# Optimization experiments

Measured on AMD Instinct MI355X. Metric: run time of the kernel, lower is better.

The kernel has to match this reference:

```python
import jax, jax.numpy as jnp
import numpy as np

D_MODEL = 768
N_HEADS = 12
HEAD_DIM = D_MODEL // N_HEADS
NEG = -10000.0


def setup_inputs() -> dict:
    key = jax.random.key(0)
    ks = jax.random.split(key, 8)
    B, S, D = 2, 2048, D_MODEL
    inp = {
        "q": jax.random.normal(ks[0], (B, S, D), dtype=jnp.float32),
        "k": jax.random.normal(ks[1], (B, S, D), dtype=jnp.float32),
        "v": jax.random.normal(ks[2], (B, S, D), dtype=jnp.float32),
        "attn_mask": jax.random.randint(ks[3], (B, S), 0, 2, dtype=jnp.int32),
        # weights stored [in, out]; apply as x @ W (equivalent to torch Linear)
        "Wq": jax.random.normal(ks[4], (D, D), dtype=jnp.float32) / np.sqrt(D),
        "Wk": jax.random.normal(ks[5], (D, D), dtype=jnp.float32) / np.sqrt(D),
        "Wv": jax.random.normal(ks[6], (D, D), dtype=jnp.float32) / np.sqrt(D),
        "Wo": jax.random.normal(ks[7], (D, D), dtype=jnp.float32) / np.sqrt(D),
        "mask_future": 1,
    }
    return inp


def reference(q, k, v, attn_mask, Wq, Wk, Wv, Wo, mask_future):
    B, S, D = q.shape
    H, hd = N_HEADS, HEAD_DIM
    # project and split heads -> [B, H, S, hd]
    qh = (q @ Wq).reshape(B, S, H, hd).transpose(0, 2, 1, 3)
    kh = (k @ Wk).reshape(B, S, H, hd).transpose(0, 2, 1, 3)
    vh = (v @ Wv).reshape(B, S, H, hd).transpose(0, 2, 1, 3)

    scale = 1.0 / np.sqrt(hd).astype(np.float32)
    # full [B, H, L, S] score matrix (naive SDPA, as in the original)
    scores = jnp.einsum("bhld,bhsd->bhls", qh, kh) * scale
    if mask_future:
        causal = jnp.triu(jnp.full((S, S), NEG, dtype=scores.dtype), k=1)
        scores = scores + causal
    # padding mask: [B, S] -> broadcast over heads and query positions
    pad = attn_mask[:, None, None, :] == 0
    scores = jnp.where(pad, NEG, scores)
    attn = jax.nn.softmax(scores, axis=-1)  # dropout p=0.0 -> identity
    out = jnp.einsum("bhls,bhsd->bhld", attn, vh)  # [B, H, L, hd]
    out = out.transpose(0, 2, 1, 3).reshape(B, S, D)
    return out @ Wo
```

## Files before the change

kernel.cpp:

```cpp
#include <hip/hip_runtime.h>


#define NEGV (-10000.0f)

typedef __attribute__((ext_vector_type(8))) short v8s;
typedef __attribute__((ext_vector_type(4))) float v4f;
typedef __attribute__((ext_vector_type(8))) unsigned short v8u;

__device__ __forceinline__ unsigned short f2bf(float f) {
  unsigned int u = __float_as_uint(f);
  u += 0x7FFFu + ((u >> 16) & 1u);
  return (unsigned short)(u >> 16);
}

__global__ __launch_bounds__(256) void transpose_w(
    const float* __restrict__ w0, const float* __restrict__ w1,
    const float* __restrict__ w2, const float* __restrict__ w3,
    unsigned short* __restrict__ t0, unsigned short* __restrict__ t1,
    unsigned short* __restrict__ t2, unsigned short* __restrict__ t3) {
  const float* w; unsigned short* t;
  switch (blockIdx.z) {
    case 0: w = w0; t = t0; break;
    case 1: w = w1; t = t1; break;
    case 2: w = w2; t = t2; break;
    default: w = w3; t = t3; break;
  }
  __shared__ unsigned short tile[32][33];
  const int tx = threadIdx.x & 31, ty = threadIdx.x >> 5;
  const int x0 = blockIdx.x * 32, y0 = blockIdx.y * 32;
#pragma unroll
  for (int j = 0; j < 4; j++)
    tile[ty + j * 8][tx] = f2bf(w[(size_t)(y0 + ty + j * 8) * 768 + x0 + tx]);
  __syncthreads();
#pragma unroll
  for (int j = 0; j < 4; j++)
    t[(size_t)(x0 + ty + j * 8) * 768 + y0 + tx] = tile[tx][ty + j * 8];
}

template <bool ABF16HEAD, bool CF32ROW>
__device__ __forceinline__ void gemm_core(const void* __restrict__ A,
                                          const unsigned short* __restrict__ Wt,
                                          void* __restrict__ C) {
  const int tid = threadIdx.x;
  const int wave = tid >> 6, lane = tid & 63;
  const int quad = lane >> 4, l16 = lane & 15;
  const int wm = wave >> 1, wn = wave & 1;
  const int bm = blockIdx.x * 128, bn = blockIdx.y * 128;

  __shared__ __align__(16) unsigned short As[128 * 32];
  __shared__ __align__(16) unsigned short Bs[128 * 32];

  v4f acc[4][4];
#pragma unroll
  for (int i = 0; i < 4; i++)
#pragma unroll
    for (int j = 0; j < 4; j++) acc[i][j] = (v4f){0.f, 0.f, 0.f, 0.f};

  for (int kt = 0; kt < 24; kt++) {
    __syncthreads();
#pragma unroll
    for (int p = 0; p < 2; p++) {
      int idx = p * 256 + tid;
      int r = idx >> 2, c0 = (idx & 3) << 3;
      int rg = bm + r, c = kt * 32 + c0;
      if (ABF16HEAD) {
        size_t aoff = ((size_t)((rg >> 11) * 12 + (c >> 6)) * 2048 +
                       (rg & 2047)) * 64 + (c & 63);
        *(uint4*)&As[r * 32 + c0] =
            *(const uint4*)((const unsigned short*)A + aoff);
      } else {
        const float* Af = (const float*)A;
        size_t aoff = (size_t)rg * 768 + c;
        float4 x0 = *(const float4*)(Af + aoff);
        float4 x1 = *(const float4*)(Af + aoff + 4);
        v8u tmp;
        tmp[0] = f2bf(x0.x); tmp[1] = f2bf(x0.y);
        tmp[2] = f2bf(x0.z); tmp[3] = f2bf(x0.w);
        tmp[4] = f2bf(x1.x); tmp[5] = f2bf(x1.y);
        tmp[6] = f2bf(x1.z); tmp[7] = f2bf(x1.w);
        *(uint4*)&As[r * 32 + c0] = *(uint4*)&tmp;
      }
      *(uint4*)&Bs[r * 32 + c0] =
          *(const uint4*)&Wt[(size_t)(bn + r) * 768 + c];
    }
    __syncthreads();

    v8s aF[4], bF[4];
#pragma unroll
    for (int mt = 0; mt < 4; mt++)
      aF[mt] = *(const v8s*)&As[(wm * 64 + mt * 16 + l16) * 32 + quad * 8];
#pragma unroll
    for (int nt = 0; nt < 4; nt++)
      bF[nt] = *(const v8s*)&Bs[(wn * 64 + nt * 16 + l16) * 32 + quad * 8];
#pragma unroll
    for (int mt = 0; mt < 4; mt++)
#pragma unroll
      for (int nt = 0; nt < 4; nt++)
        acc[mt][nt] = __builtin_amdgcn_mfma_f32_16x16x32_bf16(
            aF[mt], bF[nt], acc[mt][nt], 0, 0, 0);
  }

#pragma unroll
  for (int mt = 0; mt < 4; mt++) {
#pragma unroll
    for (int i = 0; i < 4; i++) {
      int row = bm + wm * 64 + mt * 16 + quad * 4 + i;
#pragma unroll
      for (int nt = 0; nt < 4; nt++) {
        int col = bn + wn * 64 + nt * 16 + l16;
        if (CF32ROW) {
          ((float*)C)[(size_t)row * 768 + col] = acc[mt][nt][i];
        } else {
          size_t off = ((size_t)((row >> 11) * 12 + (col >> 6)) * 2048 +
                        (row & 2047)) * 64 + (col & 63);
          ((unsigned short*)C)[off] = f2bf(acc[mt][nt][i]);
        }
      }
    }
  }
}

__global__ __launch_bounds__(256) void gemm_qkv(
    const float* __restrict__ xq, const float* __restrict__ xk,
    const float* __restrict__ xv, const unsigned short* __restrict__ wqt,
    const unsigned short* __restrict__ wkt, const unsigned short* __restrict__ wvt,
    unsigned short* __restrict__ qh, unsigned short* __restrict__ kh,
    unsigned short* __restrict__ vh) {
  const float* A; const unsigned short* Wt; unsigned short* C;
  switch (blockIdx.z) {
    case 0: A = xq; Wt = wqt; C = qh; break;
    case 1: A = xk; Wt = wkt; C = kh; break;
    default: A = xv; Wt = wvt; C = vh; break;
  }
  gemm_core<false, false>((const void*)A, Wt, (void*)C);
}

__global__ __launch_bounds__(256) void gemm_o(
    const unsigned short* __restrict__ oat, const unsigned short* __restrict__ wot,
    float* __restrict__ out) {
  gemm_core<true, true>((const void*)oat, wot, (void*)out);
}

__global__ __launch_bounds__(256) void attn_kernel(
    const unsigned short* __restrict__ qh, const unsigned short* __restrict__ kh,
    const unsigned short* __restrict__ vh, const int* __restrict__ attn_mask,
    const int* __restrict__ mask_future, unsigned short* __restrict__ o) {
  const int S = 2048, HD = 64, NH = 12;

  const int nlin = blockIdx.x + 32 * blockIdx.y;
  const int m_ = nlin & 255, t_ = nlin >> 8;
  const int i_ = (t_ == 1) ? (511 - m_) : (t_ * 256 + m_);
  const int qt = 31 - i_ / 24;
  const int bh = i_ - (i_ / 24) * 24;
  const int b = bh / NH, h = bh % NH;

  const int tid = threadIdx.x;
  const int wave = tid >> 6, lane = tid & 63;
  const int quad = lane >> 4, l16 = lane & 15;

  __shared__ __align__(16) unsigned short Ks[64 * 72];
  __shared__ __align__(16) unsigned short Vt[64 * 72];
  __shared__ __align__(16) unsigned short Ps[4][16 * 72];
  __shared__ int Ms[64];
  __shared__ int s_flag;

  const size_t head_off = (size_t)(b * NH + h) * S * HD;
  const unsigned short* Kb = kh + head_off;
  const unsigned short* Vb = vh + head_off;

  const int mf = mask_future[0];
  if (tid == 0) s_flag = 0;

  const int qrowA = qt * 64 + wave * 16 + l16;
  v8s aQ[2];
  {
    const unsigned short* qp = qh + head_off + (size_t)qrowA * HD + quad * 8;
    aQ[0] = *(const v8s*)(qp);
    aQ[1] = *(const v8s*)(qp + 32);
  }
  const int qbase = qt * 64 + wave * 16 + quad * 4;

  float m_i[4], l_i[4];
  v4f accO[4];
#pragma unroll
  for (int i = 0; i < 4; i++) { m_i[i] = -1e30f; l_i[i] = 0.f; }
#pragma unroll
  for (int dt = 0; dt < 4; dt++) accO[dt] = (v4f){0.f, 0.f, 0.f, 0.f};

  const int kt_causal = mf ? qt : (S / 64 - 1);

  uint4 pk0, pk1, pv0, pv1;
  int pm = 0;
  bool have = false;

  auto prefetch = [&](int kt) {
    const uint4* srck = (const uint4*)(Kb + (size_t)kt * 64 * HD);
    const uint4* srcv = (const uint4*)(Vb + (size_t)kt * 64 * HD);
    pk0 = srck[tid];
    pk1 = srck[256 + tid];
    pv0 = srcv[tid];
    pv1 = srcv[256 + tid];
    if (tid < 64) pm = attn_mask[b * S + kt * 64 + tid];
  };

  auto stage = [&]() {
#pragma unroll
    for (int p = 0; p < 2; p++) {
      int idx = p * 256 + tid;
      int r = idx >> 3;
      int c0 = (idx & 7) << 3;
      *(uint4*)&Ks[r * 72 + c0] = p ? pk1 : pk0;
      v8u vv;
      *(uint4*)&vv = p ? pv1 : pv0;
#pragma unroll
      for (int i = 0; i < 8; i++) {
        int d = c0 + i;
        int scol = (r + c0) & 63;
        Vt[d * 72 + scol] = vv[i];
      }
    }
    if (tid < 64) Ms[tid] = pm;
  };

  for (int phase = 0; phase < 2; phase++) {
    int kt_lo, kt_hi;
    if (phase == 0) { kt_lo = 0; kt_hi = kt_causal; }
    else {
      bool need = (m_i[0] < -5000.f) || (m_i[1] < -5000.f) ||
                  (m_i[2] < -5000.f) || (m_i[3] < -5000.f);
      if (need) s_flag = 1;
      __syncthreads();
      if (!s_flag) break;
      kt_lo = kt_causal + 1; kt_hi = S / 64 - 1;
    }
    for (int kt = kt_lo; kt <= kt_hi; kt++) {
      if (!have) prefetch(kt);
      __syncthreads();
      stage();
      __syncthreads();

      {
        int ktn = -1;
        if (kt < kt_hi) ktn = kt + 1;
        else if (phase == 0 && mf && kt_causal < S / 64 - 1)
          ktn = kt_causal + 1;
        if (ktn >= 0) { prefetch(ktn); have = true; }
        else have = false;
      }

      v4f sc[4];
      __builtin_amdgcn_s_setprio(1);
#pragma unroll
      for (int nt = 0; nt < 4; nt++) {
        const unsigned short* kp = &Ks[(nt * 16 + l16) * 72 + quad * 8];
        v8s b0 = *(const v8s*)kp;
        v8s b1 = *(const v8s*)(kp + 32);
        v4f z = (v4f){0.f, 0.f, 0.f, 0.f};
        z = __builtin_amdgcn_mfma_f32_16x16x32_bf16(aQ[0], b0, z, 0, 0, 0);
        z = __builtin_amdgcn_mfma_f32_16x16x32_bf16(aQ[1], b1, z, 0, 0, 0);
        sc[nt] = z;
      }
      __builtin_amdgcn_s_setprio(0);

#pragma unroll
      for (int nt = 0; nt < 4; nt++) {
        int key = kt * 64 + nt * 16 + l16;
        bool pad = (Ms[nt * 16 + l16] == 0);
#pragma unroll
        for (int i = 0; i < 4; i++) {
          float v = sc[nt][i] * 0.125f;
          v += (mf && (key > qbase + i)) ? NEGV : 0.f;
          v = pad ? NEGV : v;
          sc[nt][i] = v;
        }
      }

#pragma unroll
      for (int i = 0; i < 4; i++) {
        float mx = fmaxf(fmaxf(sc[0][i], sc[1][i]), fmaxf(sc[2][i], sc[3][i]));
        mx = fmaxf(mx, __shfl_xor(mx, 1));
        mx = fmaxf(mx, __shfl_xor(mx, 2));
        mx = fmaxf(mx, __shfl_xor(mx, 4));
        mx = fmaxf(mx, __shfl_xor(mx, 8));
        float mnew = fmaxf(m_i[i], mx);
        float alpha = __expf(m_i[i] - mnew);
        m_i[i] = mnew;
        float rs = 0.f;
#pragma unroll
        for (int nt = 0; nt < 4; nt++) {
          float p = __expf(sc[nt][i] - mnew);
          sc[nt][i] = p;
          rs += p;
        }
        rs += __shfl_xor(rs, 1);
        rs += __shfl_xor(rs, 2);
        rs += __shfl_xor(rs, 4);
        rs += __shfl_xor(rs, 8);
        l_i[i] = l_i[i] * alpha + rs;
#pragma unroll
        for (int dt = 0; dt < 4; dt++) accO[dt][i] *= alpha;
      }

#pragma unroll
      for (int nt = 0; nt < 4; nt++)
#pragma unroll
        for (int i = 0; i < 4; i++)
          Ps[wave][(quad * 4 + i) * 72 + nt * 16 + l16] = f2bf(sc[nt][i]);

      __builtin_amdgcn_s_setprio(1);
#pragma unroll
      for (int ks = 0; ks < 2; ks++) {
        v8s aP = *(const v8s*)&Ps[wave][l16 * 72 + ks * 32 + quad * 8];
#pragma unroll
        for (int dt = 0; dt < 4; dt++) {
          int d = dt * 16 + l16;
          int scol = ((ks * 32 + quad * 8) + ((d >> 3) << 3)) & 63;
          v8s bV = *(const v8s*)&Vt[d * 72 + scol];
          accO[dt] =
              __builtin_amdgcn_mfma_f32_16x16x32_bf16(aP, bV, accO[dt], 0, 0, 0);
        }
      }
      __builtin_amdgcn_s_setprio(0);
    }
    if (phase == 0) __syncthreads();
  }

#pragma unroll
  for (int i = 0; i < 4; i++) {
    float inv = 1.f / l_i[i];
    int qr = qbase + i;
    size_t base = head_off + (size_t)qr * HD;
#pragma unroll
    for (int dt = 0; dt < 4; dt++)
      o[base + dt * 16 + l16] = f2bf(accO[dt][i] * inv);
  }
}

extern "C" void kernel_launch(void* const* d_in, const int* in_sizes, int n_in,
                              void* d_out, int out_size, void* d_ws, size_t ws_size,
                              hipStream_t stream) {
  const float* q  = (const float*)d_in[0];
  const float* k  = (const float*)d_in[1];
  const float* v  = (const float*)d_in[2];
  const int* amask = (const int*)d_in[3];
  const float* Wq = (const float*)d_in[4];
  const float* Wk = (const float*)d_in[5];
  const float* Wv = (const float*)d_in[6];
  const float* Wo = (const float*)d_in[7];
  const int* mf  = (const int*)d_in[8];
  float* out = (float*)d_out;

  unsigned short* ws = (unsigned short*)d_ws;
  unsigned short* qh = ws;
  unsigned short* kh = qh + 3145728;
  unsigned short* vh = kh + 3145728;
  unsigned short* wqt = vh + 3145728;
  unsigned short* wkt = wqt + 589824;
  unsigned short* wvt = wkt + 589824;
  unsigned short* wot = wvt + 589824;

  transpose_w<<<dim3(24, 24, 4), 256, 0, stream>>>(Wq, Wk, Wv, Wo,
                                                   wqt, wkt, wvt, wot);
  gemm_qkv<<<dim3(32, 6, 3), 256, 0, stream>>>(q, k, v, wqt, wkt, wvt,
                                               qh, kh, vh);
  attn_kernel<<<dim3(32, 24), 256, 0, stream>>>(qh, kh, vh, amask, mf, qh);
  gemm_o<<<dim3(32, 6), 256, 0, stream>>>(qh, wot, out);
}
```

Measured before the change: 234.4 us.

## Pre-transpose V globally, compute row sums via MFMA, pack max reduction in f16

```diff
diff --git a/kernel.cpp b/kernel.cpp
--- a/kernel.cpp
+++ b/kernel.cpp
@@ -6,11 +6,18 @@
 typedef __attribute__((ext_vector_type(8))) short v8s;
 typedef __attribute__((ext_vector_type(4))) float v4f;
 typedef __attribute__((ext_vector_type(8))) unsigned short v8u;
+typedef __fp16 h2v __attribute__((ext_vector_type(2)));
 
 __device__ __forceinline__ unsigned short f2bf(float f) {
   unsigned int u = __float_as_uint(f);
   u += 0x7FFFu + ((u >> 16) & 1u);
   return (unsigned short)(u >> 16);
+}
+
+__device__ __forceinline__ int pkmax_f16(int a, int b) {
+  int r;
+  asm("v_pk_max_f16 %0, %1, %2" : "=v"(r) : "v"(a), "v"(b));
+  return r;
 }
 
 __global__ __launch_bounds__(256) void transpose_w(
@@ -35,6 +42,23 @@
 #pragma unroll
   for (int j = 0; j < 4; j++)
     t[(size_t)(x0 + ty + j * 8) * 768 + y0 + tx] = tile[tx][ty + j * 8];
+}
+
+__global__ __launch_bounds__(256) void transpose_vh(
+    const unsigned short* __restrict__ vh, unsigned short* __restrict__ vht) {
+  __shared__ unsigned short tile[32][33];
+  const size_t hoff = (size_t)blockIdx.z * 2048 * 64;
+  const unsigned short* src = vh + hoff;
+  unsigned short* dst = vht + hoff;
+  const int s0 = blockIdx.x * 32, d0 = blockIdx.y * 32;
+  const int tx = threadIdx.x & 31, ty = threadIdx.x >> 5;
+#pragma unroll
+  for (int j = 0; j < 4; j++)
+    tile[ty + j * 8][tx] = src[(size_t)(s0 + ty + j * 8) * 64 + d0 + tx];
+  __syncthreads();
+#pragma unroll
+  for (int j = 0; j < 4; j++)
+    dst[(size_t)(d0 + ty + j * 8) * 2048 + s0 + tx] = tile[tx][ty + j * 8];
 }
 
 template <bool ABF16HEAD, bool CF32ROW>
@@ -143,7 +167,7 @@
 
 __global__ __launch_bounds__(256) void attn_kernel(
     const unsigned short* __restrict__ qh, const unsigned short* __restrict__ kh,
-    const unsigned short* __restrict__ vh, const int* __restrict__ attn_mask,
+    const unsigned short* __restrict__ vht, const int* __restrict__ attn_mask,
     const int* __restrict__ mask_future, unsigned short* __restrict__ o) {
   const int S = 2048, HD = 64, NH = 12;
 
@@ -166,7 +190,7 @@
 
   const size_t head_off = (size_t)(b * NH + h) * S * HD;
   const unsigned short* Kb = kh + head_off;
-  const unsigned short* Vb = vh + head_off;
+  const unsigned short* Vb = vht + head_off;
 
   const int mf = mask_future[0];
   if (tid == 0) s_flag = 0;
@@ -180,14 +204,20 @@
   }
   const int qbase = qt * 64 + wave * 16 + quad * 4;
 
-  float m_i[4], l_i[4];
-  v4f accO[4];
-#pragma unroll
-  for (int i = 0; i < 4; i++) { m_i[i] = -1e30f; l_i[i] = 0.f; }
+  float m_i[4];
+  v4f accO[4], accL;
+#pragma unroll
+  for (int i = 0; i < 4; i++) m_i[i] = -1e30f;
+  accL = (v4f){0.f, 0.f, 0.f, 0.f};
 #pragma unroll
   for (int dt = 0; dt < 4; dt++) accO[dt] = (v4f){0.f, 0.f, 0.f, 0.f};
 
+  v8s ones;
+#pragma unroll
+  for (int j = 0; j < 8; j++) ones[j] = (short)0x3F80;
+
   const int kt_causal = mf ? qt : (S / 64 - 1);
+  const int r0 = tid >> 3, c0s = (tid & 7) << 3;
 
   uint4 pk0, pk1, pv0, pv1;
   int pm = 0;
@@ -195,30 +225,19 @@
 
   auto prefetch = [&](int kt) {
     const uint4* srck = (const uint4*)(Kb + (size_t)kt * 64 * HD);
-    const uint4* srcv = (const uint4*)(Vb + (size_t)kt * 64 * HD);
     pk0 = srck[tid];
     pk1 = srck[256 + tid];
-    pv0 = srcv[tid];
-    pv1 = srcv[256 + tid];
+    const unsigned short* vp = Vb + (size_t)r0 * S + kt * 64 + c0s;
+    pv0 = *(const uint4*)vp;
+    pv1 = *(const uint4*)(vp + (size_t)32 * S);
     if (tid < 64) pm = attn_mask[b * S + kt * 64 + tid];
   };
 
   auto stage = [&]() {
-#pragma unroll
-    for (int p = 0; p < 2; p++) {
-      int idx = p * 256 + tid;
-      int r = idx >> 3;
-      int c0 = (idx & 7) << 3;
-      *(uint4*)&Ks[r * 72 + c0] = p ? pk1 : pk0;
-      v8u vv;
-      *(uint4*)&vv = p ? pv1 : pv0;
-#pragma unroll
-      for (int i = 0; i < 8; i++) {
-        int d = c0 + i;
-        int scol = (r + c0) & 63;
-        Vt[d * 72 + scol] = vv[i];
-      }
-    }
+    *(uint4*)&Ks[r0 * 72 + c0s] = pk0;
+    *(uint4*)&Ks[(r0 + 32) * 72 + c0s] = pk1;
+    *(uint4*)&Vt[r0 * 72 + c0s] = pv0;
+    *(uint4*)&Vt[(r0 + 32) * 72 + c0s] = pv1;
     if (tid < 64) Ms[tid] = pm;
   };
 
@@ -275,30 +294,35 @@
         }
       }
 
+      float m4[4];
+#pragma unroll
+      for (int i = 0; i < 4; i++)
+        m4[i] = fmaxf(fmaxf(sc[0][i], sc[1][i]), fmaxf(sc[2][i], sc[3][i]));
+      union { h2v h; int v; } pk01, pk23;
+      pk01.h = __builtin_amdgcn_cvt_pkrtz(m4[0], m4[1]);
+      pk23.h = __builtin_amdgcn_cvt_pkrtz(m4[2], m4[3]);
+      int v01 = pk01.v, v23 = pk23.v;
+#pragma unroll
+      for (int mk = 1; mk <= 8; mk <<= 1) {
+        v01 = pkmax_f16(v01, __shfl_xor(v01, mk));
+        v23 = pkmax_f16(v23, __shfl_xor(v23, mk));
+      }
+      union { int v; h2v h; } u01, u23;
+      u01.v = v01; u23.v = v23;
+      float mx[4] = {(float)u01.h[0], (float)u01.h[1],
+                     (float)u23.h[0], (float)u23.h[1]};
+
 #pragma unroll
       for (int i = 0; i < 4; i++) {
-        float mx = fmaxf(fmaxf(sc[0][i], sc[1][i]), fmaxf(sc[2][i], sc[3][i]));
-        mx = fmaxf(mx, __shfl_xor(mx, 1));
-        mx = fmaxf(mx, __shfl_xor(mx, 2));
-        mx = fmaxf(mx, __shfl_xor(mx, 4));
-        mx = fmaxf(mx, __shfl_xor(mx, 8));
-        float mnew = fmaxf(m_i[i], mx);
+        float mnew = fmaxf(m_i[i], mx[i]);
         float alpha = __expf(m_i[i] - mnew);
         m_i[i] = mnew;
-        float rs = 0.f;
-#pragma unroll
-        for (int nt = 0; nt < 4; nt++) {
-          float p = __expf(sc[nt][i] - mnew);
-          sc[nt][i] = p;
-          rs += p;
-        }
-        rs += __shfl_xor(rs, 1);
-        rs += __shfl_xor(rs, 2);
-        rs += __shfl_xor(rs, 4);
-        rs += __shfl_xor(rs, 8);
-        l_i[i] = l_i[i] * alpha + rs;
+#pragma unroll
+        for (int nt = 0; nt < 4; nt++)
+          sc[nt][i] = __expf(sc[nt][i] - mnew);
 #pragma unroll
         for (int dt = 0; dt < 4; dt++) accO[dt][i] *= alpha;
+        accL[i] *= alpha;
       }
 
 #pragma unroll
@@ -311,11 +335,10 @@
 #pragma unroll
       for (int ks = 0; ks < 2; ks++) {
         v8s aP = *(const v8s*)&Ps[wave][l16 * 72 + ks * 32 + quad * 8];
+        accL = __builtin_amdgcn_mfma_f32_16x16x32_bf16(aP, ones, accL, 0, 0, 0);
 #pragma unroll
         for (int dt = 0; dt < 4; dt++) {
-          int d = dt * 16 + l16;
-          int scol = ((ks * 32 + quad * 8) + ((d >> 3) << 3)) & 63;
-          v8s bV = *(const v8s*)&Vt[d * 72 + scol];
+          v8s bV = *(const v8s*)&Vt[(dt * 16 + l16) * 72 + ks * 32 + quad * 8];
           accO[dt] =
               __builtin_amdgcn_mfma_f32_16x16x32_bf16(aP, bV, accO[dt], 0, 0, 0);
         }
@@ -327,7 +350,7 @@
 
 #pragma unroll
   for (int i = 0; i < 4; i++) {
-    float inv = 1.f / l_i[i];
+    float inv = 1.f / accL[i];
     int qr = qbase + i;
     size_t base = head_off + (size_t)qr * HD;
 #pragma unroll
@@ -358,11 +381,13 @@
   unsigned short* wkt = wqt + 589824;
   unsigned short* wvt = wkt + 589824;
   unsigned short* wot = wvt + 589824;
+  unsigned short* vht = (unsigned short*)d_out;
 
   transpose_w<<<dim3(24, 24, 4), 256, 0, stream>>>(Wq, Wk, Wv, Wo,
                                                    wqt, wkt, wvt, wot);
   gemm_qkv<<<dim3(32, 6, 3), 256, 0, stream>>>(q, k, v, wqt, wkt, wvt,
                                                qh, kh, vh);
-  attn_kernel<<<dim3(32, 24), 256, 0, stream>>>(qh, kh, vh, amask, mf, qh);
+  transpose_vh<<<dim3(64, 2, 24), 256, 0, stream>>>(vh, vht);
+  attn_kernel<<<dim3(32, 24), 256, 0, stream>>>(qh, kh, vht, amask, mf, qh);
   gemm_o<<<dim3(32, 6), 256, 0, stream>>>(qh, wot, out);
 }
```

After: 221.5 us. -5.5%, faster.
